# Optimization experiments

Hardware: AMD Instinct MI355X
Metric: run time of the kernel (lower is better)

Reference implementation:

```python
import jax, jax.numpy as jnp
import numpy as np

N_NODES = 50000
N_EDGES = 800000
IN_FEATS = 128
H_FEATS = 128
NUM_CLASSES = 64


def _linear_params(key, fan_in, fan_out):
    kw, kb = jax.random.split(key)
    bound = 1.0 / np.sqrt(fan_in)
    W = jax.random.uniform(kw, (fan_out, fan_in), minval=-bound, maxval=bound, dtype=jnp.float32)
    b = jax.random.uniform(kb, (fan_out,), minval=-bound, maxval=bound, dtype=jnp.float32)
    return W, b


def setup_inputs() -> dict:
    key = jax.random.key(0)
    k_feat, k_src, k_dst, k1, k2, k3 = jax.random.split(key, 6)
    in_feat = jax.random.normal(k_feat, (N_NODES, IN_FEATS), dtype=jnp.float32)
    src = jax.random.randint(k_src, (N_EDGES,), 0, N_NODES, dtype=jnp.int32)
    dst = jax.random.randint(k_dst, (N_EDGES,), 0, N_NODES, dtype=jnp.int32)
    W1, b1 = _linear_params(k1, IN_FEATS, H_FEATS)
    W2, b2 = _linear_params(k2, H_FEATS, H_FEATS)
    W3, b3 = _linear_params(k3, H_FEATS, NUM_CLASSES)
    return {"in_feat": in_feat, "W1": W1, "b1": b1, "W2": W2, "b2": b2,
            "W3": W3, "b3": b3, "src": src, "dst": dst}


def reference(in_feat, W1, b1, W2, b2, W3, b3, src, dst):
    N = in_feat.shape[0]

    def gin_layer(x, W, b):
        # DGL GINConv with eps=0: (x + sum of in-neighbor messages) -> Linear
        agg = jax.ops.segment_sum(x[src], dst, num_segments=N)  # [N, d]
        return jax.nn.relu((x + agg) @ W.T + b)

    h = gin_layer(in_feat, W1, b1)
    h = gin_layer(h, W2, b2)
    h = gin_layer(h, W3, b3)
    return h
```

## Files before the change

### kernel.cpp

```cpp
#include <hip/hip_runtime.h>

typedef _Float16 half8 __attribute__((ext_vector_type(8)));
typedef _Float16 half2v __attribute__((ext_vector_type(2)));
typedef float floatx4 __attribute__((ext_vector_type(4)));
typedef unsigned int uintx4 __attribute__((ext_vector_type(4)));

union AB { uint4 u; half8 h; };
union H2 { unsigned int u; _Float16 h[2]; };
union H2P { unsigned int u; half2v h; };
union US16 { uintx4 u[2]; unsigned short s[16]; };

#define CAPLOG 6
#define CAP 64

__global__ __launch_bounds__(256) void histA_init_k(
    const int* __restrict__ dst, int* __restrict__ histG, int E, int nbins,
    const float* __restrict__ F, const float* __restrict__ W1,
    const float* __restrict__ W2, const float* __restrict__ W3,
    _Float16* __restrict__ hX, _Float16* __restrict__ W1h,
    _Float16* __restrict__ W2h, _Float16* __restrict__ W3h,
    _Float16* __restrict__ hZ,
    int n4f, int n4w1, int n4w2, int n4w3, int zoffX4, int zoffZ4) {
    int t = threadIdx.x;
    if (blockIdx.x < 256) {
        __shared__ int h[256];
        h[t] = 0;
        __syncthreads();
        int per = (E + 255) / 256;
        int beg = blockIdx.x * per;
        int end = min(E, beg + per);
        for (int e = beg + t; e < end; e += 256)
            atomicAdd(&h[dst[e] >> 8], 1);
        __syncthreads();
        for (int i = t; i < nbins; i += 256)
            histG[i * 256 + blockIdx.x] = h[i];
        return;
    }
    int i = (blockIdx.x - 256) * 256 + t;
    const float* X;
    _Float16* O;
    int j;
    if (i < n4f) { X = F; O = hX; j = i; }
    else if (i < n4f + n4w1) { X = W1; O = W1h; j = i - n4f; }
    else if (i < n4f + n4w1 + n4w2) { X = W2; O = W2h; j = i - n4f - n4w1; }
    else if (i < n4f + n4w1 + n4w2 + n4w3) { X = W3; O = W3h; j = i - n4f - n4w1 - n4w2; }
    else {
        int z = i - (n4f + n4w1 + n4w2 + n4w3);
        if (z < 16) ((uint4*)hX)[zoffX4 + z] = make_uint4(0, 0, 0, 0);
        else if (z < 24) ((uint4*)hZ)[zoffZ4 + (z - 16)] = make_uint4(0, 0, 0, 0);
        return;
    }
    float4 v = reinterpret_cast<const float4*>(X)[j];
    union { uint2 u; _Float16 h[4]; } o;
    o.h[0] = (_Float16)v.x; o.h[1] = (_Float16)v.y;
    o.h[2] = (_Float16)v.z; o.h[3] = (_Float16)v.w;
    reinterpret_cast<uint2*>(O)[j] = o.u;
}

__global__ __launch_bounds__(1024) void scan1_k(const int* __restrict__ x,
                                                int* __restrict__ inc,
                                                int* __restrict__ partial, int n) {
    __shared__ int sd[1024];
    int t = threadIdx.x;
    int v = blockIdx.x * 1024 + t;
    sd[t] = (v < n) ? x[v] : 0;
    __syncthreads();
    for (int off = 1; off < 1024; off <<= 1) {
        int val = (t >= off) ? sd[t - off] : 0;
        __syncthreads();
        sd[t] += val;
        __syncthreads();
    }
    if (v < n) inc[v] = sd[t];
    if (t == 1023) partial[blockIdx.x] = sd[1023];
}

__global__ __launch_bounds__(256) void scatterB_k(const int* __restrict__ src,
                                                  const int* __restrict__ dst,
                                                  const int* __restrict__ inc,
                                                  const int* __restrict__ histG,
                                                  const int* __restrict__ partial, int nparts,
                                                  unsigned int* __restrict__ binned,
                                                  int E, int nbins) {
    __shared__ int cur[256];
    __shared__ int pp[64];
    int t = threadIdx.x, blk = blockIdx.x;
    if (t < 64) {
        int v = (t < nparts) ? partial[t] : 0;
        for (int off = 1; off < 64; off <<= 1) {
            int n = __shfl_up(v, off, 64);
            if (t >= off) v += n;
        }
        int ex = __shfl_up(v, 1, 64);
        if (t == 0) ex = 0;
        pp[t] = ex;
    }
    __syncthreads();
    for (int i = t; i < nbins; i += 256) {
        int idx = i * 256 + blk;
        cur[i] = inc[idx] + pp[idx >> 10] - histG[idx];
    }
    __syncthreads();
    int per = (E + 255) / 256;
    int beg = blk * per;
    int end = min(E, beg + per);
    for (int e = beg + t; e < end; e += 256) {
        int d = dst[e];
        int s = src[e];
        int pos = atomicAdd(&cur[d >> 8], 1);
        binned[pos] = ((unsigned int)(d & 255) << 16) | (unsigned int)s;
    }
}

__global__ __launch_bounds__(256) void binB_k(const unsigned int* __restrict__ binned,
                                              const int* __restrict__ inc,
                                              const int* __restrict__ histG,
                                              const int* __restrict__ partial, int nparts,
                                              unsigned short* __restrict__ col,
                                              int* __restrict__ cnt,
                                              int N, int E, int nbins) {
    __shared__ unsigned short lcol[256 * CAP];
    __shared__ int lcnt[256];
    __shared__ int pp[64];
    __shared__ int bounds[2];
    int t = threadIdx.x;
    int b = blockIdx.x;
    if (t < 64) {
        int v = (t < nparts) ? partial[t] : 0;
        for (int off = 1; off < 64; off <<= 1) {
            int n = __shfl_up(v, off, 64);
            if (t >= off) v += n;
        }
        int ex = __shfl_up(v, 1, 64);
        if (t == 0) ex = 0;
        pp[t] = ex;
    }
    unsigned int* lcol32 = (unsigned int*)lcol;
    for (int i = t; i < 256 * CAP / 2; i += 256) lcol32[i] = 0xFFFFFFFFu;
    lcnt[t] = 0;
    __syncthreads();
    if (t == 0) {
        int i0 = b * 256;
        bounds[0] = inc[i0] + pp[i0 >> 10] - histG[i0];
    } else if (t == 1) {
        if (b == nbins - 1) bounds[1] = E;
        else {
            int i1 = (b + 1) * 256;
            bounds[1] = inc[i1] + pp[i1 >> 10] - histG[i1];
        }
    }
    __syncthreads();
    int beg = bounds[0], end = bounds[1];
    for (int e = beg + t; e < end; e += 256) {
        unsigned int u = binned[e];
        int dl = u >> 16;
        int pos = atomicAdd(&lcnt[dl], 1);
        if (pos < CAP) lcol[(dl << CAPLOG) + pos] = (unsigned short)(u & 0xFFFFu);
    }
    __syncthreads();
    int base = b << 8;
    int nodes = min(256, N - base);
    uint4* colg = (uint4*)(col + ((size_t)base << CAPLOG));
    const uint4* coll = (const uint4*)lcol;
    for (int i = t; i < nodes * 8; i += 256) colg[i] = coll[i];
    for (int i = t; i < nodes; i += 256) cnt[base + i] = lcnt[i];
}

__global__ __launch_bounds__(256) void aggregate_k(const _Float16* __restrict__ X,
                                                   const int* __restrict__ cnt,
                                                   const unsigned short* __restrict__ col,
                                                   _Float16* __restrict__ Y,
                                                   int nnodes) {
    int w = blockIdx.x * 4 + (threadIdx.x >> 6);
    int lane = threadIdx.x & 63;
    if (w >= nnodes) return;
    const unsigned int* X32 = reinterpret_cast<const unsigned int*>(X);
    int deg = cnt[w];
    if (deg > CAP) deg = CAP;
    int degp = (deg + 15) & ~15;
    const unsigned short* c = col + ((size_t)w << CAPLOG);

    H2P acc[16];
#pragma unroll
    for (int j = 0; j < 16; j++) acc[j].u = 0u;

    for (int e = 0; e < degp; e += 16) {
        US16 ix;
        ix.u[0] = *reinterpret_cast<const uintx4*>(c + e);
        ix.u[1] = *reinterpret_cast<const uintx4*>(c + e + 8);
        H2P u[16];
#pragma unroll
        for (int j = 0; j < 16; j++) {
            int s = (int)ix.s[j];
            s = (s < nnodes) ? s : nnodes;
            u[j].u = X32[(size_t)s * 64 + lane];
        }
#pragma unroll
        for (int j = 0; j < 16; j++) acc[j].h += u[j].h;
    }

    float s0 = 0.f, s1 = 0.f;
#pragma unroll
    for (int j = 0; j < 16; j++) {
        s0 += (float)acc[j].h[0];
        s1 += (float)acc[j].h[1];
    }
    H2 xs, r;
    xs.u = X32[(size_t)w * 64 + lane];
    r.h[0] = (_Float16)((float)xs.h[0] + s0);
    r.h[1] = (_Float16)((float)xs.h[1] + s1);
    __builtin_nontemporal_store(r.u, reinterpret_cast<unsigned int*>(Y) + (size_t)w * 64 + lane);
}

__global__ __launch_bounds__(256) void agg_final_k(const _Float16* __restrict__ Z,
                                                   const int* __restrict__ cnt,
                                                   const unsigned short* __restrict__ col,
                                                   const float* __restrict__ bias,
                                                   float* __restrict__ out, int nnodes) {
    int lane = threadIdx.x & 63;
    int fl = lane & 31;
    int node = blockIdx.x * 8 + (threadIdx.x >> 6) * 2 + (lane >> 5);
    if (node >= nnodes) return;
    const unsigned int* Z32 = (const unsigned int*)Z;

    int deg = cnt[node];
    if (deg > CAP) deg = CAP;
    int degp = (deg + 15) & ~15;
    const unsigned short* c = col + ((size_t)node << CAPLOG);

    H2P acc[16];
#pragma unroll
    for (int j = 0; j < 16; j++) acc[j].u = 0u;

    for (int e = 0; e < degp; e += 16) {
        US16 ix;
        ix.u[0] = *reinterpret_cast<const uintx4*>(c + e);
        ix.u[1] = *reinterpret_cast<const uintx4*>(c + e + 8);
        H2P u[16];
#pragma unroll
        for (int j = 0; j < 16; j++) {
            int s = (int)ix.s[j];
            s = (s < nnodes) ? s : nnodes;
            u[j].u = Z32[(size_t)s * 32 + fl];
        }
#pragma unroll
        for (int j = 0; j < 16; j++) acc[j].h += u[j].h;
    }

    float s0 = 0.f, s1 = 0.f;
#pragma unroll
    for (int j = 0; j < 16; j++) {
        s0 += (float)acc[j].h[0];
        s1 += (float)acc[j].h[1];
    }
    H2 xs;
    xs.u = Z32[(size_t)node * 32 + fl];
    float2 bv = reinterpret_cast<const float2*>(bias)[fl];
    float2 r;
    r.x = fmaxf((float)xs.h[0] + s0 + bv.x, 0.f);
    r.y = fmaxf((float)xs.h[1] + s1 + bv.y, 0.f);
    reinterpret_cast<float2*>(out)[(size_t)node * 32 + fl] = r;
}

template <int NOUT, bool RAW>
__global__ __launch_bounds__(256) void gemm_mfma_k(const _Float16* __restrict__ Y,
                                                   const _Float16* __restrict__ Wh,
                                                   const float* __restrict__ bias,
                                                   _Float16* __restrict__ out, int nnodes) {
    constexpr int NT = NOUT / 16;
    constexpr int WSTR = 136;
    __shared__ _Float16 Wl[NOUT * WSTR];
    __shared__ float Bl[NOUT];

    const int t = threadIdx.x;
    for (int p = t; p < NOUT * 16; p += 256) {
        int f = p >> 4;
        int kq = (p & 15) * 8;
        uint4 u = *reinterpret_cast<const uint4*>(Wh + f * 128 + kq);
        *reinterpret_cast<uint4*>(&Wl[f * WSTR + kq]) = u;
    }
    if (!RAW && t < NOUT) Bl[t] = bias[t];
    __syncthreads();

    const int wave = t >> 6;
    const int lane = t & 63;
    const int quad = lane >> 4;
    const int fcol = lane & 15;
    const int m_base = (blockIdx.x * 4 + wave) * 16;
    const int row = m_base + fcol;
    const bool rowok = row < nnodes;

    floatx4 acc[NT];
#pragma unroll
    for (int ft = 0; ft < NT; ft++) acc[ft] = (floatx4){0.f, 0.f, 0.f, 0.f};

    const uint4* Yrow = reinterpret_cast<const uint4*>(Y + (size_t)row * 128);
#pragma unroll
    for (int step = 0; step < 4; step++) {
        AB a;
        if (rowok) a.u = Yrow[step * 4 + quad];
        else       a.u = make_uint4(0u, 0u, 0u, 0u);
#pragma unroll
        for (int ft = 0; ft < NT; ft++) {
            half8 b = *reinterpret_cast<const half8*>(
                &Wl[(ft * 16 + fcol) * WSTR + step * 32 + quad * 8]);
            acc[ft] = __builtin_amdgcn_mfma_f32_16x16x32_f16(a.h, b, acc[ft], 0, 0, 0);
        }
    }

#pragma unroll
    for (int ft = 0; ft < NT; ft++) {
        int f = ft * 16 + fcol;
        float bv = RAW ? 0.f : Bl[f];
#pragma unroll
        for (int r = 0; r < 4; r++) {
            int node = m_base + quad * 4 + r;
            if (node < nnodes) {
                float v = acc[ft][r] + bv;
                if (!RAW) v = fmaxf(v, 0.f);
                out[(size_t)node * NOUT + f] = (_Float16)v;
            }
        }
    }
}

extern "C" void kernel_launch(void* const* d_in, const int* in_sizes, int n_in,
                              void* d_out, int out_size, void* d_ws, size_t ws_size,
                              hipStream_t stream) {
    const float* in_feat = (const float*)d_in[0];
    const float* W1 = (const float*)d_in[1];
    const float* b1 = (const float*)d_in[2];
    const float* W2 = (const float*)d_in[3];
    const float* b2 = (const float*)d_in[4];
    const float* W3 = (const float*)d_in[5];
    const float* b3 = (const float*)d_in[6];
    const int* src = (const int*)d_in[7];
    const int* dst = (const int*)d_in[8];
    float* out = (float*)d_out;

    const int N = in_sizes[0] / 128;
    const int E = in_sizes[7];
    const int szW1 = in_sizes[1];
    const int szW2 = in_sizes[3];
    const int szW3 = in_sizes[5];
    const int nbins = (N + 255) >> 8;
    const int nhist = nbins * 256;

    char* p = (char*)d_ws;
    int* cnt = (int*)p;               p += (size_t)N * 4;
    unsigned short* col = (unsigned short*)p; p += (size_t)N * CAP * 2;
    int* histG = (int*)p;             p += (size_t)nhist * 4;
    int* incS = (int*)p;              p += (size_t)nhist * 4;
    int* partial = (int*)p;           p += 256;
    unsigned int* binned = (unsigned int*)p; p += (size_t)E * 4;
    _Float16* hX = (_Float16*)p;      p += (size_t)(N + 1) * 128 * 2;
    _Float16* hB = (_Float16*)p;      p += (size_t)N * 128 * 2;
    _Float16* hZ = (_Float16*)p;      p += (size_t)(N + 1) * 64 * 2;
    _Float16* W1h = (_Float16*)p;     p += (size_t)szW1 * 2;
    _Float16* W2h = (_Float16*)p;     p += (size_t)szW2 * 2;
    _Float16* W3h = (_Float16*)p;     p += (size_t)szW3 * 2;

    const int nblk_scan = (nhist + 1023) / 1024;

    {
        int n4f = N * 128 / 4;
        int total = n4f + szW1 / 4 + szW2 / 4 + szW3 / 4 + 32;
        int iblk = (total + 255) / 256;
        histA_init_k<<<256 + iblk, 256, 0, stream>>>(dst, histG, E, nbins,
                                                     in_feat, W1, W2, W3,
                                                     hX, W1h, W2h, W3h, hZ,
                                                     n4f, szW1 / 4, szW2 / 4, szW3 / 4,
                                                     N * 16, N * 8);
    }
    scan1_k<<<nblk_scan, 1024, 0, stream>>>(histG, incS, partial, nhist);
    scatterB_k<<<256, 256, 0, stream>>>(src, dst, incS, histG, partial, nblk_scan,
                                        binned, E, nbins);
    binB_k<<<nbins, 256, 0, stream>>>(binned, incS, histG, partial, nblk_scan,
                                      col, cnt, N, E, nbins);

    const int nblk_agg = (N + 3) / 4;
    const int nblk_gemm = (N + 63) / 64;
    aggregate_k<<<nblk_agg, 256, 0, stream>>>(hX, cnt, col, hB, N);
    gemm_mfma_k<128, false><<<nblk_gemm, 256, 0, stream>>>(hB, W1h, b1, hX, N);
    aggregate_k<<<nblk_agg, 256, 0, stream>>>(hX, cnt, col, hB, N);
    gemm_mfma_k<128, false><<<nblk_gemm, 256, 0, stream>>>(hB, W2h, b2, hX, N);
    gemm_mfma_k<64, true><<<nblk_gemm, 256, 0, stream>>>(hX, W3h, nullptr, hZ, N);
    agg_final_k<<<(N + 7) / 8, 256, 0, stream>>>(hZ, cnt, col, b3, out, N);
}
```

Baseline: 238.7 us.

## Fuse layer-2 and layer-3 GEMMs and process two nodes per wave in aggregation

Merges the layer-2 GEMM (with bias and ReLU) and the raw layer-3 projection into one kernel. The intermediate 128-wide activations stay in shared memory, so they are never written to or read back from global memory, and one launch is removed. The aggregation kernels now handle two destination nodes per wave (or half-wave), putting twice as many gathers in flight. The cost is higher register and LDS use, plus wasted gathers when the two paired nodes have very different degrees.

```diff
diff --git a/kernel.cpp b/kernel.cpp
--- a/kernel.cpp
+++ b/kernel.cpp
@@ -171,45 +171,65 @@
                                                    const unsigned short* __restrict__ col,
                                                    _Float16* __restrict__ Y,
                                                    int nnodes) {
-    int w = blockIdx.x * 4 + (threadIdx.x >> 6);
+    int wA = blockIdx.x * 8 + (threadIdx.x >> 6) * 2;
     int lane = threadIdx.x & 63;
-    if (w >= nnodes) return;
+    if (wA >= nnodes) return;
+    int wB = wA + 1;
+    bool hasB = (wB < nnodes);
     const unsigned int* X32 = reinterpret_cast<const unsigned int*>(X);
-    int deg = cnt[w];
-    if (deg > CAP) deg = CAP;
-    int degp = (deg + 15) & ~15;
-    const unsigned short* c = col + ((size_t)w << CAPLOG);
-
-    H2P acc[16];
-#pragma unroll
-    for (int j = 0; j < 16; j++) acc[j].u = 0u;
+    int degA = min(cnt[wA], CAP);
+    int degB = hasB ? min(cnt[wB], CAP) : 0;
+    int degp = (max(degA, degB) + 15) & ~15;
+    const unsigned short* cA = col + ((size_t)wA << CAPLOG);
+    const unsigned short* cB = col + ((size_t)(hasB ? wB : wA) << CAPLOG);
+
+    H2P accA[8], accB[8];
+#pragma unroll
+    for (int j = 0; j < 8; j++) { accA[j].u = 0u; accB[j].u = 0u; }
 
     for (int e = 0; e < degp; e += 16) {
-        US16 ix;
-        ix.u[0] = *reinterpret_cast<const uintx4*>(c + e);
-        ix.u[1] = *reinterpret_cast<const uintx4*>(c + e + 8);
-        H2P u[16];
+        US16 ixA, ixB;
+        ixA.u[0] = *reinterpret_cast<const uintx4*>(cA + e);
+        ixA.u[1] = *reinterpret_cast<const uintx4*>(cA + e + 8);
+        ixB.u[0] = *reinterpret_cast<const uintx4*>(cB + e);
+        ixB.u[1] = *reinterpret_cast<const uintx4*>(cB + e + 8);
+        H2P uA[16], uB[16];
 #pragma unroll
         for (int j = 0; j < 16; j++) {
-            int s = (int)ix.s[j];
-            s = (s < nnodes) ? s : nnodes;
-            u[j].u = X32[(size_t)s * 64 + lane];
-        }
-#pragma unroll
-        for (int j = 0; j < 16; j++) acc[j].h += u[j].h;
-    }
-
-    float s0 = 0.f, s1 = 0.f;
-#pragma unroll
-    for (int j = 0; j < 16; j++) {
-        s0 += (float)acc[j].h[0];
-        s1 += (float)acc[j].h[1];
-    }
-    H2 xs, r;
-    xs.u = X32[(size_t)w * 64 + lane];
-    r.h[0] = (_Float16)((float)xs.h[0] + s0);
-    r.h[1] = (_Float16)((float)xs.h[1] + s1);
-    __builtin_nontemporal_store(r.u, reinterpret_cast<unsigned int*>(Y) + (size_t)w * 64 + lane);
+            int sA = (int)ixA.s[j];
+            sA = (sA < nnodes) ? sA : nnodes;
+            uA[j].u = X32[(size_t)sA * 64 + lane];
+            int sB = (int)ixB.s[j];
+            sB = (sB < nnodes) ? sB : nnodes;
+            uB[j].u = X32[(size_t)sB * 64 + lane];
+        }
+#pragma unroll
+        for (int j = 0; j < 8; j++) {
+            accA[j].h += uA[j].h;
+            accA[j].h += uA[j + 8].h;
+            accB[j].h += uB[j].h;
+            accB[j].h += uB[j + 8].h;
+        }
+    }
+
+    float a0 = 0.f, a1 = 0.f, b0 = 0.f, b1 = 0.f;
+#pragma unroll
+    for (int j = 0; j < 8; j++) {
+        a0 += (float)accA[j].h[0]; a1 += (float)accA[j].h[1];
+        b0 += (float)accB[j].h[0]; b1 += (float)accB[j].h[1];
+    }
+    H2 xsA, rA;
+    xsA.u = X32[(size_t)wA * 64 + lane];
+    rA.h[0] = (_Float16)((float)xsA.h[0] + a0);
+    rA.h[1] = (_Float16)((float)xsA.h[1] + a1);
+    __builtin_nontemporal_store(rA.u, reinterpret_cast<unsigned int*>(Y) + (size_t)wA * 64 + lane);
+    if (hasB) {
+        H2 xsB, rB;
+        xsB.u = X32[(size_t)wB * 64 + lane];
+        rB.h[0] = (_Float16)((float)xsB.h[0] + b0);
+        rB.h[1] = (_Float16)((float)xsB.h[1] + b1);
+        __builtin_nontemporal_store(rB.u, reinterpret_cast<unsigned int*>(Y) + (size_t)wB * 64 + lane);
+    }
 }
 
 __global__ __launch_bounds__(256) void agg_final_k(const _Float16* __restrict__ Z,
@@ -219,67 +239,86 @@
                                                    float* __restrict__ out, int nnodes) {
     int lane = threadIdx.x & 63;
     int fl = lane & 31;
-    int node = blockIdx.x * 8 + (threadIdx.x >> 6) * 2 + (lane >> 5);
-    if (node >= nnodes) return;
+    int nA = blockIdx.x * 16 + (threadIdx.x >> 6) * 4 + (lane >> 5) * 2;
+    if (nA >= nnodes) return;
+    int nB = nA + 1;
+    bool hasB = (nB < nnodes);
     const unsigned int* Z32 = (const unsigned int*)Z;
-
-    int deg = cnt[node];
-    if (deg > CAP) deg = CAP;
-    int degp = (deg + 15) & ~15;
-    const unsigned short* c = col + ((size_t)node << CAPLOG);
-
-    H2P acc[16];
-#pragma unroll
-    for (int j = 0; j < 16; j++) acc[j].u = 0u;
+    int degA = min(cnt[nA], CAP);
+    int degB = hasB ? min(cnt[nB], CAP) : 0;
+    int degp = (max(degA, degB) + 15) & ~15;
+    const unsigned short* cA = col + ((size_t)nA << CAPLOG);
+    const unsigned short* cB = col + ((size_t)(hasB ? nB : nA) << CAPLOG);
+
+    H2P accA[8], accB[8];
+#pragma unroll
+    for (int j = 0; j < 8; j++) { accA[j].u = 0u; accB[j].u = 0u; }
 
     for (int e = 0; e < degp; e += 16) {
-        US16 ix;
-        ix.u[0] = *reinterpret_cast<const uintx4*>(c + e);
-        ix.u[1] = *reinterpret_cast<const uintx4*>(c + e + 8);
-        H2P u[16];
+        US16 ixA, ixB;
+        ixA.u[0] = *reinterpret_cast<const uintx4*>(cA + e);
+        ixA.u[1] = *reinterpret_cast<const uintx4*>(cA + e + 8);
+        ixB.u[0] = *reinterpret_cast<const uintx4*>(cB + e);
+        ixB.u[1] = *reinterpret_cast<const uintx4*>(cB + e + 8);
+        H2P uA[16], uB[16];
 #pragma unroll
         for (int j = 0; j < 16; j++) {
-            int s = (int)ix.s[j];
-            s = (s < nnodes) ? s : nnodes;
-            u[j].u = Z32[(size_t)s * 32 + fl];
-        }
-#pragma unroll
-        for (int j = 0; j < 16; j++) acc[j].h += u[j].h;
-    }
-
-    float s0 = 0.f, s1 = 0.f;
-#pragma unroll
-    for (int j = 0; j < 16; j++) {
-        s0 += (float)acc[j].h[0];
-        s1 += (float)acc[j].h[1];
-    }
-    H2 xs;
-    xs.u = Z32[(size_t)node * 32 + fl];
+            int sA = (int)ixA.s[j];
+            sA = (sA < nnodes) ? sA : nnodes;
+            uA[j].u = Z32[(size_t)sA * 32 + fl];
+            int sB = (int)ixB.s[j];
+            sB = (sB < nnodes) ? sB : nnodes;
+            uB[j].u = Z32[(size_t)sB * 32 + fl];
+        }
+#pragma unroll
+        for (int j = 0; j < 8; j++) {
+            accA[j].h += uA[j].h;
+            accA[j].h += uA[j + 8].h;
+            accB[j].h += uB[j].h;
+            accB[j].h += uB[j + 8].h;
+        }
+    }
+
+    float a0 = 0.f, a1 = 0.f, b0 = 0.f, b1 = 0.f;
+#pragma unroll
+    for (int j = 0; j < 8; j++) {
+        a0 += (float)accA[j].h[0]; a1 += (float)accA[j].h[1];
+        b0 += (float)accB[j].h[0]; b1 += (float)accB[j].h[1];
+    }
     float2 bv = reinterpret_cast<const float2*>(bias)[fl];
-    float2 r;
-    r.x = fmaxf((float)xs.h[0] + s0 + bv.x, 0.f);
-    r.y = fmaxf((float)xs.h[1] + s1 + bv.y, 0.f);
-    reinterpret_cast<float2*>(out)[(size_t)node * 32 + fl] = r;
-}
-
-template <int NOUT, bool RAW>
+    H2 xsA;
+    xsA.u = Z32[(size_t)nA * 32 + fl];
+    float2 rA;
+    rA.x = fmaxf((float)xsA.h[0] + a0 + bv.x, 0.f);
+    rA.y = fmaxf((float)xsA.h[1] + a1 + bv.y, 0.f);
+    reinterpret_cast<float2*>(out)[(size_t)nA * 32 + fl] = rA;
+    if (hasB) {
+        H2 xsB;
+        xsB.u = Z32[(size_t)nB * 32 + fl];
+        float2 rB;
+        rB.x = fmaxf((float)xsB.h[0] + b0 + bv.x, 0.f);
+        rB.y = fmaxf((float)xsB.h[1] + b1 + bv.y, 0.f);
+        reinterpret_cast<float2*>(out)[(size_t)nB * 32 + fl] = rB;
+    }
+}
+
 __global__ __launch_bounds__(256) void gemm_mfma_k(const _Float16* __restrict__ Y,
                                                    const _Float16* __restrict__ Wh,
                                                    const float* __restrict__ bias,
                                                    _Float16* __restrict__ out, int nnodes) {
-    constexpr int NT = NOUT / 16;
+    constexpr int NT = 8;
     constexpr int WSTR = 136;
-    __shared__ _Float16 Wl[NOUT * WSTR];
-    __shared__ float Bl[NOUT];
+    __shared__ _Float16 Wl[128 * WSTR];
+    __shared__ float Bl[128];
 
     const int t = threadIdx.x;
-    for (int p = t; p < NOUT * 16; p += 256) {
+    for (int p = t; p < 128 * 16; p += 256) {
         int f = p >> 4;
         int kq = (p & 15) * 8;
-        uint4 u = *reinterpret_cast<const uint4*>(Wh + f * 128 + kq);
-        *reinterpret_cast<uint4*>(&Wl[f * WSTR + kq]) = u;
-    }
-    if (!RAW && t < NOUT) Bl[t] = bias[t];
+        *reinterpret_cast<uint4*>(&Wl[f * WSTR + kq]) =
+            *reinterpret_cast<const uint4*>(Wh + f * 128 + kq);
+    }
+    if (t < 128) Bl[t] = bias[t];
     __syncthreads();
 
     const int wave = t >> 6;
@@ -311,15 +350,105 @@
 #pragma unroll
     for (int ft = 0; ft < NT; ft++) {
         int f = ft * 16 + fcol;
-        float bv = RAW ? 0.f : Bl[f];
+        float bv = Bl[f];
 #pragma unroll
         for (int r = 0; r < 4; r++) {
             int node = m_base + quad * 4 + r;
-            if (node < nnodes) {
-                float v = acc[ft][r] + bv;
-                if (!RAW) v = fmaxf(v, 0.f);
-                out[(size_t)node * NOUT + f] = (_Float16)v;
-            }
+            if (node < nnodes)
+                out[(size_t)node * 128 + f] = (_Float16)fmaxf(acc[ft][r] + bv, 0.f);
+        }
+    }
+}
+
+__global__ __launch_bounds__(256) void gemm23_k(const _Float16* __restrict__ Y,
+                                                const _Float16* __restrict__ W2h,
+                                                const float* __restrict__ b2,
+                                                const _Float16* __restrict__ W3h,
+                                                _Float16* __restrict__ hZ, int nnodes) {
+    constexpr int WSTR = 136;
+    __shared__ _Float16 Wl[128 * WSTR];
+    __shared__ _Float16 Hl[64 * WSTR];
+    __shared__ float Bl[128];
+
+    const int t = threadIdx.x;
+    for (int p = t; p < 128 * 16; p += 256) {
+        int f = p >> 4;
+        int kq = (p & 15) * 8;
+        *reinterpret_cast<uint4*>(&Wl[f * WSTR + kq]) =
+            *reinterpret_cast<const uint4*>(W2h + f * 128 + kq);
+    }
+    if (t < 128) Bl[t] = b2[t];
+    __syncthreads();
+
+    const int wave = t >> 6;
+    const int lane = t & 63;
+    const int quad = lane >> 4;
+    const int fcol = lane & 15;
+    const int m_base = (blockIdx.x * 4 + wave) * 16;
+    const int row = m_base + fcol;
+    const bool rowok = row < nnodes;
+
+    floatx4 acc[8];
+#pragma unroll
+    for (int ft = 0; ft < 8; ft++) acc[ft] = (floatx4){0.f, 0.f, 0.f, 0.f};
+
+    const uint4* Yrow = reinterpret_cast<const uint4*>(Y + (size_t)row * 128);
+#pragma unroll
+    for (int step = 0; step < 4; step++) {
+        AB a;
+        if (rowok) a.u = Yrow[step * 4 + quad];
+        else       a.u = make_uint4(0u, 0u, 0u, 0u);
+#pragma unroll
+        for (int ft = 0; ft < 8; ft++) {
+            half8 b = *reinterpret_cast<const half8*>(
+                &Wl[(ft * 16 + fcol) * WSTR + step * 32 + quad * 8]);
+            acc[ft] = __builtin_amdgcn_mfma_f32_16x16x32_f16(a.h, b, acc[ft], 0, 0, 0);
+        }
+    }
+
+#pragma unroll
+    for (int ft = 0; ft < 8; ft++) {
+        int f = ft * 16 + fcol;
+        float bv = Bl[f];
+#pragma unroll
+        for (int r = 0; r < 4; r++) {
+            int nl = wave * 16 + quad * 4 + r;
+            Hl[nl * WSTR + f] = (_Float16)fmaxf(acc[ft][r] + bv, 0.f);
+        }
+    }
+    __syncthreads();
+
+    for (int p = t; p < 64 * 16; p += 256) {
+        int f = p >> 4;
+        int kq = (p & 15) * 8;
+        *reinterpret_cast<uint4*>(&Wl[f * WSTR + kq]) =
+            *reinterpret_cast<const uint4*>(W3h + f * 128 + kq);
+    }
+    __syncthreads();
+
+    floatx4 acc2[4];
+#pragma unroll
+    for (int ft = 0; ft < 4; ft++) acc2[ft] = (floatx4){0.f, 0.f, 0.f, 0.f};
+#pragma unroll
+    for (int step = 0; step < 4; step++) {
+        AB a;
+        a.h = *reinterpret_cast<const half8*>(
+            &Hl[(wave * 16 + fcol) * WSTR + step * 32 + quad * 8]);
+#pragma unroll
+        for (int ft = 0; ft < 4; ft++) {
+            half8 b = *reinterpret_cast<const half8*>(
+                &Wl[(ft * 16 + fcol) * WSTR + step * 32 + quad * 8]);
+            acc2[ft] = __builtin_amdgcn_mfma_f32_16x16x32_f16(a.h, b, acc2[ft], 0, 0, 0);
+        }
+    }
+#pragma unroll
+    for (int ft = 0; ft < 4; ft++) {
+        int f = ft * 16 + fcol;
+#pragma unroll
+        for (int r = 0; r < 4; r++) {
+            int node = m_base + quad * 4 + r;
+            if (node < nnodes)
+                hZ[(size_t)node * 64 + f] = (_Float16)acc2[ft][r];
         }
     }
 }
@@ -378,12 +507,11 @@
     binB_k<<<nbins, 256, 0, stream>>>(binned, incS, histG, partial, nblk_scan,
                                       col, cnt, N, E, nbins);
 
-    const int nblk_agg = (N + 3) / 4;
+    const int nblk_agg = (N + 7) / 8;
     const int nblk_gemm = (N + 63) / 64;
     aggregate_k<<<nblk_agg, 256, 0, stream>>>(hX, cnt, col, hB, N);
-    gemm_mfma_k<128, false><<<nblk_gemm, 256, 0, stream>>>(hB, W1h, b1, hX, N);
+    gemm_mfma_k<<<nblk_gemm, 256, 0, stream>>>(hB, W1h, b1, hX, N);
     aggregate_k<<<nblk_agg, 256, 0, stream>>>(hX, cnt, col, hB, N);
-    gemm_mfma_k<128, false><<<nblk_gemm, 256, 0, stream>>>(hB, W2h, b2, hX, N);
-    gemm_mfma_k<64, true><<<nblk_gemm, 256, 0, stream>>>(hX, W3h, nullptr, hZ, N);
-    agg_final_k<<<(N + 7) / 8, 256, 0, stream>>>(hZ, cnt, col, b3, out, N);
-}
+    gemm23_k<<<nblk_gemm, 256, 0, stream>>>(hB, W2h, b2, W3h, hZ, N);
+    agg_final_k<<<(N + 15) / 16, 256, 0, stream>>>(hZ, cnt, col, b3, out, N);
+}
```

New measurement: 239.2 us. About the same (+0.2%).
